# Optimization experiments

Measured on AMD Instinct MI355X. Metric: run time of the kernel, lower is better.

The kernel has to match this reference:

```python
import jax, jax.numpy as jnp
import numpy as np

NUM_USERS = 50000
NUM_ITEMS = 50000
N_NODES = NUM_USERS + NUM_ITEMS
EMBED_DIM = 64
NUM_LAYERS = 2
NUM_EDGES = 3200000


def setup_inputs() -> dict:
    key = jax.random.key(0)
    ks = jax.random.split(key, 8)
    edge_index = jax.random.randint(ks[0], (2, NUM_EDGES), 0, N_NODES, dtype=jnp.int32)
    edge_weight = jax.random.uniform(ks[1], (NUM_EDGES,), dtype=jnp.float32)
    scale = 1.0 / np.sqrt(EMBED_DIM)
    user_emb = jax.random.normal(ks[2], (NUM_USERS, EMBED_DIM), dtype=jnp.float32)
    item_emb = jax.random.normal(ks[3], (NUM_ITEMS, EMBED_DIM), dtype=jnp.float32)
    W1 = jax.random.normal(ks[4], (EMBED_DIM, EMBED_DIM), dtype=jnp.float32) * scale
    b1 = jnp.zeros((EMBED_DIM,), dtype=jnp.float32)
    W2 = jax.random.normal(ks[5], (EMBED_DIM, EMBED_DIM), dtype=jnp.float32) * scale
    b2 = jnp.zeros((EMBED_DIM,), dtype=jnp.float32)
    return {"edge_index": edge_index, "edge_weight": edge_weight,
            "user_emb": user_emb, "item_emb": item_emb,
            "W1": W1, "b1": b1, "W2": W2, "b2": b2}


def _gcn_layer(x, edge_index, edge_weight, W, b):
    # message: x_j * w_e ; aggregate: scatter-add to target nodes
    src, dst = edge_index[0], edge_index[1]
    msgs = x[src] * edge_weight[:, None]              # [E, D]
    agg = jax.ops.segment_sum(msgs, dst, num_segments=N_NODES)  # [N, D]
    updated = (agg + x) * 0.5                          # residual average
    return updated @ W.T + b                           # nn.Linear


def reference(edge_index, edge_weight, user_emb, item_emb, W1, b1, W2, b2):
    x = jnp.concatenate([user_emb, item_emb], axis=0)  # [N, D]
    x = _gcn_layer(x, edge_index, edge_weight, W1, b1)
    x = _gcn_layer(x, edge_index, edge_weight, W2, b2)
    return x
```

## Files before the change

kernel.cpp:

```cpp
#include <hip/hip_runtime.h>

#define N_NODES 100000
#define NUM_U 50000
#define D 64
#define NUM_E 3200000
#define NB 391
#define PBLK 256
#define CHUNK (NUM_E / PBLK)

__device__ __forceinline__ float bf2f(unsigned short u) {
  return __uint_as_float((unsigned)u << 16);
}
__device__ __forceinline__ unsigned short f2bf(float f) {
  unsigned u = __float_as_uint(f);
  u += 0x7FFF + ((u >> 16) & 1);
  return (unsigned short)(u >> 16);
}

__global__ __launch_bounds__(256) void micro_kernel(
    const float* __restrict__ W1, const float* __restrict__ W2,
    const float* __restrict__ b1, const float* __restrict__ b2,
    float* __restrict__ M, float* __restrict__ c, float* __restrict__ cc) {
  __shared__ float w1[64][65], w2[64][65];
  int t = (int)threadIdx.x;
  for (int i = t; i < 4096; i += 256) { w1[i >> 6][i & 63] = W1[i]; w2[i >> 6][i & 63] = W2[i]; }
  __syncthreads();
  for (int i = t; i < 4096; i += 256) {
    int k = i >> 6, j = i & 63;
    float s = 0.f;
#pragma unroll
    for (int tt = 0; tt < 64; ++tt) s = fmaf(w2[j][tt], w1[tt][k], s);
    M[i] = s;
  }
  if (t < 64) {
    float s = 0.f;
#pragma unroll
    for (int tt = 0; tt < 64; ++tt) s = fmaf(b1[tt], w2[t][tt], s);
    c[t] = s;
    cc[t] = 0.5f * s + b2[t];
  }
}

__global__ __launch_bounds__(256) void zmm_kernel(
    const float* __restrict__ xu, const float* __restrict__ xi,
    const float* __restrict__ M, unsigned short* __restrict__ z16) {
  __shared__ float Mt[64][65];
  __shared__ float U[64][65];
  int t = (int)threadIdx.x;
  for (int i = t; i < 4096; i += 256) Mt[i & 63][i >> 6] = M[i];
  int lane = t & 63, row = t >> 6;
  int n0 = (int)blockIdx.x * 64;
#pragma unroll
  for (int i = 0; i < 16; ++i) {
    int nl = row + 4 * i, n = n0 + nl;
    if (n < N_NODES) {
      const float* xr = (n < NUM_U) ? (xu + (size_t)n * D) : (xi + (size_t)(n - NUM_U) * D);
      U[nl][lane] = xr[lane];
    }
  }
  __syncthreads();
#pragma unroll
  for (int i = 0; i < 16; ++i) {
    int nl = row + 4 * i, n = n0 + nl;
    if (n >= N_NODES) continue;
    float s = 0.f;
#pragma unroll
    for (int k = 0; k < 64; ++k) s = fmaf(U[nl][k], Mt[lane][k], s);
    z16[(size_t)n * D + lane] = f2bf(s);
  }
}

__global__ __launch_bounds__(256) void p1_hist(const int4* __restrict__ dst4,
                                               int* __restrict__ gcnt,
                                               int* __restrict__ tot) {
  __shared__ int h[NB];
  int t = (int)threadIdx.x, blk = (int)blockIdx.x;
  for (int i = t; i < NB; i += 256) h[i] = 0;
  __syncthreads();
  int base4 = blk * (CHUNK / 4);
  for (int i = t; i < CHUNK / 4; i += 256) {
    int4 d = dst4[base4 + i];
    atomicAdd(&h[d.x >> 8], 1); atomicAdd(&h[d.y >> 8], 1);
    atomicAdd(&h[d.z >> 8], 1); atomicAdd(&h[d.w >> 8], 1);
  }
  __syncthreads();
  for (int i = t; i < NB; i += 256) {
    gcnt[i * PBLK + blk] = h[i];
    atomicAdd(&tot[i], h[i]);
  }
}

__global__ __launch_bounds__(512) void p2_scan(const int* __restrict__ tot,
                                               int* __restrict__ bbase,
                                               int* __restrict__ rowptr) {
  __shared__ int ps[512];
  int t = (int)threadIdx.x;
  int v = (t < NB) ? tot[t] : 0;
  ps[t] = v;
  __syncthreads();
  for (int off = 1; off < 512; off <<= 1) {
    int a = (t >= off) ? ps[t - off] : 0;
    __syncthreads();
    ps[t] += a;
    __syncthreads();
  }
  if (t < NB) bbase[t] = ps[t] - v;
  if (t == 0) { bbase[NB] = NUM_E; rowptr[N_NODES] = NUM_E; }
}

__global__ __launch_bounds__(256) void p2_off(const int* __restrict__ gcnt,
                                              const int* __restrict__ bbase,
                                              int* __restrict__ off) {
  __shared__ int ps[256];
  int t = (int)threadIdx.x, b = (int)blockIdx.x;
  int v = gcnt[b * PBLK + t];
  ps[t] = v;
  __syncthreads();
  for (int o = 1; o < 256; o <<= 1) {
    int a = (t >= o) ? ps[t - o] : 0;
    __syncthreads();
    ps[t] += a;
    __syncthreads();
  }
  off[b * PBLK + t] = bbase[b] + ps[t] - v;
}

__global__ __launch_bounds__(256) void p3_part(const int4* __restrict__ src4,
                                               const int4* __restrict__ dst4,
                                               const float4* __restrict__ w4,
                                               const int* __restrict__ off,
                                               int2* __restrict__ staging) {
  __shared__ int cur[NB];
  int t = (int)threadIdx.x, blk = (int)blockIdx.x;
  for (int i = t; i < NB; i += 256) cur[i] = off[i * PBLK + blk];
  __syncthreads();
  int base4 = blk * (CHUNK / 4);
  for (int i = t; i < CHUNK / 4; i += 256) {
    int4 s = src4[base4 + i];
    int4 d = dst4[base4 + i];
    float4 w = w4[base4 + i];
    int p;
    p = atomicAdd(&cur[d.x >> 8], 1);
    staging[p] = make_int2(s.x | ((d.x & 255) << 17), __float_as_int(w.x));
    p = atomicAdd(&cur[d.y >> 8], 1);
    staging[p] = make_int2(s.y | ((d.y & 255) << 17), __float_as_int(w.y));
    p = atomicAdd(&cur[d.z >> 8], 1);
    staging[p] = make_int2(s.z | ((d.z & 255) << 17), __float_as_int(w.z));
    p = atomicAdd(&cur[d.w >> 8], 1);
    staging[p] = make_int2(s.w | ((d.w & 255) << 17), __float_as_int(w.w));
  }
}

__global__ __launch_bounds__(256) void csr_finalize(
    const int* __restrict__ bbase, const int2* __restrict__ staging,
    int2* __restrict__ meta, int* __restrict__ rowptr) {
  __shared__ int hist[256];
  __shared__ int ps[256];
  __shared__ int cur[256];
  int t = (int)threadIdx.x, b = (int)blockIdx.x;
  int bs = bbase[b], be = bbase[b + 1];
  hist[t] = 0;
  __syncthreads();
  for (int i = bs + t; i < be; i += 256) atomicAdd(&hist[staging[i].x >> 17], 1);
  __syncthreads();
  int v = hist[t];
  ps[t] = v;
  __syncthreads();
  for (int o = 1; o < 256; o <<= 1) {
    int a = (t >= o) ? ps[t - o] : 0;
    __syncthreads();
    ps[t] += a;
    __syncthreads();
  }
  int base = bs + ps[t] - v;
  cur[t] = base;
  int n = b * 256 + t;
  if (n < N_NODES) rowptr[n] = base;
  __syncthreads();
  for (int i = bs + t; i < be; i += 256) {
    int2 m = staging[i];
    int dl = m.x >> 17;
    int p = atomicAdd(&cur[dl], 1);
    meta[p] = make_int2(m.x & 0x1FFFF, m.y);
  }
}

template <bool FINAL>
__global__ __launch_bounds__(256) void gather_kernel(
    const int* __restrict__ rowptr, const int2* __restrict__ meta,
    const unsigned short* __restrict__ gsrc, const unsigned short* __restrict__ z16,
    const float* __restrict__ c, const float* __restrict__ cc,
    float* __restrict__ outf, unsigned short* __restrict__ out16) {
  int t = (int)threadIdx.x, lane = t & 63;
  int wid = (int)((blockIdx.x * blockDim.x + t) >> 6);
  int nw = (int)((gridDim.x * blockDim.x) >> 6);
  float cl = FINAL ? c[lane] : 0.f;
  float ccl = FINAL ? cc[lane] : 0.f;

  for (int n = wid; n < N_NODES; n += nw) {
    int lo = __builtin_amdgcn_readfirstlane(rowptr[n]);
    int hi = __builtin_amdgcn_readfirstlane(rowptr[n + 1]);
    float acc0 = 0.f, acc1 = 0.f, wsum = 0.f;
    int j = lo;
    for (; j + 8 <= hi; j += 8) {
      int2 m0 = meta[j + 0], m1 = meta[j + 1], m2 = meta[j + 2], m3 = meta[j + 3];
      int2 m4 = meta[j + 4], m5 = meta[j + 5], m6 = meta[j + 6], m7 = meta[j + 7];
      float v0 = bf2f(gsrc[((size_t)m0.x << 6) + lane]);
      float v1 = bf2f(gsrc[((size_t)m1.x << 6) + lane]);
      float v2 = bf2f(gsrc[((size_t)m2.x << 6) + lane]);
      float v3 = bf2f(gsrc[((size_t)m3.x << 6) + lane]);
      float v4 = bf2f(gsrc[((size_t)m4.x << 6) + lane]);
      float v5 = bf2f(gsrc[((size_t)m5.x << 6) + lane]);
      float v6 = bf2f(gsrc[((size_t)m6.x << 6) + lane]);
      float v7 = bf2f(gsrc[((size_t)m7.x << 6) + lane]);
      acc0 = fmaf(v0, __int_as_float(m0.y), acc0);
      acc1 = fmaf(v1, __int_as_float(m1.y), acc1);
      acc0 = fmaf(v2, __int_as_float(m2.y), acc0);
      acc1 = fmaf(v3, __int_as_float(m3.y), acc1);
      acc0 = fmaf(v4, __int_as_float(m4.y), acc0);
      acc1 = fmaf(v5, __int_as_float(m5.y), acc1);
      acc0 = fmaf(v6, __int_as_float(m6.y), acc0);
      acc1 = fmaf(v7, __int_as_float(m7.y), acc1);
      if (FINAL) {
        float wa = (__int_as_float(m0.y) + __int_as_float(m1.y)) +
                   (__int_as_float(m2.y) + __int_as_float(m3.y));
        float wb = (__int_as_float(m4.y) + __int_as_float(m5.y)) +
                   (__int_as_float(m6.y) + __int_as_float(m7.y));
        wsum += wa + wb;
      }
    }
    for (; j < hi; ++j) {
      int2 m = meta[j];
      acc0 = fmaf(bf2f(gsrc[((size_t)m.x << 6) + lane]), __int_as_float(m.y), acc0);
      if (FINAL) wsum += __int_as_float(m.y);
    }
    float acc = acc0 + acc1;
    size_t o = ((size_t)n << 6) + lane;
    if (FINAL) {
      float t1n = bf2f(gsrc[o]);
      float zn = bf2f(z16[o]);
      outf[o] = 0.25f * acc + 0.5f * t1n + 0.25f * zn + 0.5f * wsum * cl + ccl;
    } else {
      out16[o] = f2bf(acc);
    }
  }
}

extern "C" void kernel_launch(void* const* d_in, const int* in_sizes, int n_in,
                              void* d_out, int out_size, void* d_ws, size_t ws_size,
                              hipStream_t stream) {
  const int* edge_index = (const int*)d_in[0];
  const int* src = edge_index;
  const int* dst = edge_index + NUM_E;
  const float* w = (const float*)d_in[1];
  const float* user_emb = (const float*)d_in[2];
  const float* item_emb = (const float*)d_in[3];
  const float* W1 = (const float*)d_in[4];
  const float* b1 = (const float*)d_in[5];
  const float* W2 = (const float*)d_in[6];
  const float* b2 = (const float*)d_in[7];
  float* out = (float*)d_out;

  unsigned short* z16 = (unsigned short*)d_ws;
  int2* staging = (int2*)(z16 + (size_t)N_NODES * D);
  unsigned short* t1_16 = (unsigned short*)staging;
  int2* meta = staging + NUM_E;
  int* rowptr = (int*)(meta + NUM_E);
  int* gcnt = rowptr + 100352;
  int* off = gcnt + NB * PBLK;
  int* tot = off + NB * PBLK;
  int* bbase = tot + 392;
  float* Mbuf = (float*)(bbase + 392);
  float* cbuf = Mbuf + 4096;
  float* ccbuf = cbuf + 64;

  hipMemsetAsync(tot, 0, NB * sizeof(int), stream);

  micro_kernel<<<1, 256, 0, stream>>>(W1, W2, b1, b2, Mbuf, cbuf, ccbuf);
  zmm_kernel<<<(N_NODES + 63) / 64, 256, 0, stream>>>(user_emb, item_emb, Mbuf, z16);

  p1_hist<<<PBLK, 256, 0, stream>>>((const int4*)dst, gcnt, tot);
  p2_scan<<<1, 512, 0, stream>>>(tot, bbase, rowptr);
  p2_off<<<NB, 256, 0, stream>>>(gcnt, bbase, off);
  p3_part<<<PBLK, 256, 0, stream>>>((const int4*)src, (const int4*)dst,
                                    (const float4*)w, off, staging);
  csr_finalize<<<NB, 256, 0, stream>>>(bbase, staging, meta, rowptr);

  gather_kernel<false><<<2048, 256, 0, stream>>>(rowptr, meta, z16, z16, cbuf,
                                                 ccbuf, nullptr, t1_16);
  gather_kernel<true><<<2048, 256, 0, stream>>>(rowptr, meta, t1_16, z16, cbuf,
                                                ccbuf, out, nullptr);
}
```

Measured before the change: 415.0 us.

## Stage partition and CSR scatter through LDS, drop per-block offset scan

The partition kernel now builds a local histogram and scan per block, sorts its chunk into shared memory, reserves global bucket ranges through atomic cursors, and writes contiguous runs to staging. This replaces the separate per-block count matrix and its offset-scan kernel. csr_finalize also sorts each bucket in LDS when it fits, then writes meta coalesced. The gather loop is unrolled to 16 loads in flight. The change removes scattered global writes and one kernel launch, at the cost of heavy LDS use per block (lower occupancy) and nondeterministic edge order within buckets.

```diff
diff --git a/kernel.cpp b/kernel.cpp
--- a/kernel.cpp
+++ b/kernel.cpp
@@ -5,8 +5,10 @@
 #define D 64
 #define NUM_E 3200000
 #define NB 391
-#define PBLK 256
+#define PBLK 500
 #define CHUNK (NUM_E / PBLK)
+#define CHUNK4 (CHUNK / 4)
+#define FCAP 8928
 
 __device__ __forceinline__ float bf2f(unsigned short u) {
   return __uint_as_float((unsigned)u << 16);
@@ -71,94 +73,108 @@
 }
 
 __global__ __launch_bounds__(256) void p1_hist(const int4* __restrict__ dst4,
-                                               int* __restrict__ gcnt,
                                                int* __restrict__ tot) {
   __shared__ int h[NB];
   int t = (int)threadIdx.x, blk = (int)blockIdx.x;
   for (int i = t; i < NB; i += 256) h[i] = 0;
   __syncthreads();
-  int base4 = blk * (CHUNK / 4);
-  for (int i = t; i < CHUNK / 4; i += 256) {
+  int base4 = blk * CHUNK4;
+  for (int i = t; i < CHUNK4; i += 256) {
     int4 d = dst4[base4 + i];
     atomicAdd(&h[d.x >> 8], 1); atomicAdd(&h[d.y >> 8], 1);
     atomicAdd(&h[d.z >> 8], 1); atomicAdd(&h[d.w >> 8], 1);
   }
   __syncthreads();
-  for (int i = t; i < NB; i += 256) {
-    gcnt[i * PBLK + blk] = h[i];
-    atomicAdd(&tot[i], h[i]);
-  }
+  for (int i = t; i < NB; i += 256)
+    if (h[i]) atomicAdd(&tot[i], h[i]);
 }
 
 __global__ __launch_bounds__(512) void p2_scan(const int* __restrict__ tot,
                                                int* __restrict__ bbase,
+                                               int* __restrict__ gcursor,
                                                int* __restrict__ rowptr) {
   __shared__ int ps[512];
   int t = (int)threadIdx.x;
   int v = (t < NB) ? tot[t] : 0;
   ps[t] = v;
   __syncthreads();
-  for (int off = 1; off < 512; off <<= 1) {
-    int a = (t >= off) ? ps[t - off] : 0;
+  for (int o = 1; o < 512; o <<= 1) {
+    int a = (t >= o) ? ps[t - o] : 0;
     __syncthreads();
     ps[t] += a;
     __syncthreads();
   }
-  if (t < NB) bbase[t] = ps[t] - v;
+  if (t < NB) { int e = ps[t] - v; bbase[t] = e; gcursor[t] = e; }
   if (t == 0) { bbase[NB] = NUM_E; rowptr[N_NODES] = NUM_E; }
 }
 
-__global__ __launch_bounds__(256) void p2_off(const int* __restrict__ gcnt,
-                                              const int* __restrict__ bbase,
-                                              int* __restrict__ off) {
-  __shared__ int ps[256];
-  int t = (int)threadIdx.x, b = (int)blockIdx.x;
-  int v = gcnt[b * PBLK + t];
-  ps[t] = v;
-  __syncthreads();
-  for (int o = 1; o < 256; o <<= 1) {
-    int a = (t >= o) ? ps[t - o] : 0;
-    __syncthreads();
-    ps[t] += a;
-    __syncthreads();
-  }
-  off[b * PBLK + t] = bbase[b] + ps[t] - v;
-}
-
-__global__ __launch_bounds__(256) void p3_part(const int4* __restrict__ src4,
+__global__ __launch_bounds__(512) void p3_part(const int4* __restrict__ src4,
                                                const int4* __restrict__ dst4,
                                                const float4* __restrict__ w4,
-                                               const int* __restrict__ off,
+                                               int* __restrict__ gcursor,
                                                int2* __restrict__ staging) {
-  __shared__ int cur[NB];
+  __shared__ int2 ent[CHUNK];
+  __shared__ int h[NB];
+  __shared__ int lst[NB + 1];
+  __shared__ int og[NB];
+  __shared__ int ps[512];
   int t = (int)threadIdx.x, blk = (int)blockIdx.x;
-  for (int i = t; i < NB; i += 256) cur[i] = off[i * PBLK + blk];
-  __syncthreads();
-  int base4 = blk * (CHUNK / 4);
-  for (int i = t; i < CHUNK / 4; i += 256) {
+  for (int i = t; i < NB; i += 512) h[i] = 0;
+  __syncthreads();
+  int base4 = blk * CHUNK4;
+  for (int i = t; i < CHUNK4; i += 512) {
+    int4 d = dst4[base4 + i];
+    atomicAdd(&h[d.x >> 8], 1); atomicAdd(&h[d.y >> 8], 1);
+    atomicAdd(&h[d.z >> 8], 1); atomicAdd(&h[d.w >> 8], 1);
+  }
+  __syncthreads();
+  int v = (t < NB) ? h[t] : 0;
+  ps[t] = v;
+  __syncthreads();
+  for (int o = 1; o < 512; o <<= 1) {
+    int a = (t >= o) ? ps[t - o] : 0;
+    __syncthreads();
+    ps[t] += a;
+    __syncthreads();
+  }
+  if (t < NB) {
+    lst[t] = ps[t] - v;
+    og[t] = v ? atomicAdd(&gcursor[t], v) : 0;
+  }
+  if (t == 0) lst[NB] = CHUNK;
+  __syncthreads();
+  if (t < NB) h[t] = lst[t];
+  __syncthreads();
+  for (int i = t; i < CHUNK4; i += 512) {
     int4 s = src4[base4 + i];
     int4 d = dst4[base4 + i];
     float4 w = w4[base4 + i];
     int p;
-    p = atomicAdd(&cur[d.x >> 8], 1);
-    staging[p] = make_int2(s.x | ((d.x & 255) << 17), __float_as_int(w.x));
-    p = atomicAdd(&cur[d.y >> 8], 1);
-    staging[p] = make_int2(s.y | ((d.y & 255) << 17), __float_as_int(w.y));
-    p = atomicAdd(&cur[d.z >> 8], 1);
-    staging[p] = make_int2(s.z | ((d.z & 255) << 17), __float_as_int(w.z));
-    p = atomicAdd(&cur[d.w >> 8], 1);
-    staging[p] = make_int2(s.w | ((d.w & 255) << 17), __float_as_int(w.w));
+    p = atomicAdd(&h[d.x >> 8], 1);
+    ent[p] = make_int2(s.x | ((d.x & 255) << 17), __float_as_int(w.x));
+    p = atomicAdd(&h[d.y >> 8], 1);
+    ent[p] = make_int2(s.y | ((d.y & 255) << 17), __float_as_int(w.y));
+    p = atomicAdd(&h[d.z >> 8], 1);
+    ent[p] = make_int2(s.z | ((d.z & 255) << 17), __float_as_int(w.z));
+    p = atomicAdd(&h[d.w >> 8], 1);
+    ent[p] = make_int2(s.w | ((d.w & 255) << 17), __float_as_int(w.w));
+  }
+  __syncthreads();
+  for (int i = t; i < CHUNK; i += 512) {
+    int lo = 0, hi = NB;
+    while (hi - lo > 1) { int mid = (lo + hi) >> 1; if (lst[mid] <= i) lo = mid; else hi = mid; }
+    staging[og[lo] + (i - lst[lo])] = ent[i];
   }
 }
 
 __global__ __launch_bounds__(256) void csr_finalize(
     const int* __restrict__ bbase, const int2* __restrict__ staging,
     int2* __restrict__ meta, int* __restrict__ rowptr) {
-  __shared__ int hist[256];
-  __shared__ int ps[256];
-  __shared__ int cur[256];
+  __shared__ int2 ent[FCAP];
+  __shared__ int hist[256], ps[256], cur[256];
   int t = (int)threadIdx.x, b = (int)blockIdx.x;
   int bs = bbase[b], be = bbase[b + 1];
+  int cnt = be - bs;
   hist[t] = 0;
   __syncthreads();
   for (int i = bs + t; i < be; i += 256) atomicAdd(&hist[staging[i].x >> 17], 1);
@@ -172,16 +188,27 @@
     ps[t] += a;
     __syncthreads();
   }
-  int base = bs + ps[t] - v;
-  cur[t] = base;
+  int lexcl = ps[t] - v;
   int n = b * 256 + t;
-  if (n < N_NODES) rowptr[n] = base;
-  __syncthreads();
-  for (int i = bs + t; i < be; i += 256) {
-    int2 m = staging[i];
-    int dl = m.x >> 17;
-    int p = atomicAdd(&cur[dl], 1);
-    meta[p] = make_int2(m.x & 0x1FFFF, m.y);
+  if (n < N_NODES) rowptr[n] = bs + lexcl;
+  if (cnt <= FCAP) {
+    cur[t] = lexcl;
+    __syncthreads();
+    for (int i = bs + t; i < be; i += 256) {
+      int2 m = staging[i];
+      int p = atomicAdd(&cur[m.x >> 17], 1);
+      ent[p] = make_int2(m.x & 0x1FFFF, m.y);
+    }
+    __syncthreads();
+    for (int i = t; i < cnt; i += 256) meta[bs + i] = ent[i];
+  } else {
+    cur[t] = bs + lexcl;
+    __syncthreads();
+    for (int i = bs + t; i < be; i += 256) {
+      int2 m = staging[i];
+      int p = atomicAdd(&cur[m.x >> 17], 1);
+      meta[p] = make_int2(m.x & 0x1FFFF, m.y);
+    }
   }
 }
 
@@ -202,32 +229,41 @@
     int hi = __builtin_amdgcn_readfirstlane(rowptr[n + 1]);
     float acc0 = 0.f, acc1 = 0.f, wsum = 0.f;
     int j = lo;
-    for (; j + 8 <= hi; j += 8) {
+    for (; j + 16 <= hi; j += 16) {
+      int2 mm[16];
+      float vv[16];
+#pragma unroll
+      for (int q = 0; q < 16; ++q) mm[q] = meta[j + q];
+#pragma unroll
+      for (int q = 0; q < 16; ++q) vv[q] = bf2f(gsrc[((size_t)mm[q].x << 6) + lane]);
+#pragma unroll
+      for (int q = 0; q < 16; ++q) {
+        if (q & 1) acc1 = fmaf(vv[q], __int_as_float(mm[q].y), acc1);
+        else       acc0 = fmaf(vv[q], __int_as_float(mm[q].y), acc0);
+      }
+      if (FINAL) {
+        float s0 = 0.f, s1 = 0.f;
+#pragma unroll
+        for (int q = 0; q < 16; q += 2) {
+          s0 += __int_as_float(mm[q].y);
+          s1 += __int_as_float(mm[q + 1].y);
+        }
+        wsum += s0 + s1;
+      }
+    }
+    for (; j + 4 <= hi; j += 4) {
       int2 m0 = meta[j + 0], m1 = meta[j + 1], m2 = meta[j + 2], m3 = meta[j + 3];
-      int2 m4 = meta[j + 4], m5 = meta[j + 5], m6 = meta[j + 6], m7 = meta[j + 7];
       float v0 = bf2f(gsrc[((size_t)m0.x << 6) + lane]);
       float v1 = bf2f(gsrc[((size_t)m1.x << 6) + lane]);
       float v2 = bf2f(gsrc[((size_t)m2.x << 6) + lane]);
       float v3 = bf2f(gsrc[((size_t)m3.x << 6) + lane]);
-      float v4 = bf2f(gsrc[((size_t)m4.x << 6) + lane]);
-      float v5 = bf2f(gsrc[((size_t)m5.x << 6) + lane]);
-      float v6 = bf2f(gsrc[((size_t)m6.x << 6) + lane]);
-      float v7 = bf2f(gsrc[((size_t)m7.x << 6) + lane]);
       acc0 = fmaf(v0, __int_as_float(m0.y), acc0);
       acc1 = fmaf(v1, __int_as_float(m1.y), acc1);
       acc0 = fmaf(v2, __int_as_float(m2.y), acc0);
       acc1 = fmaf(v3, __int_as_float(m3.y), acc1);
-      acc0 = fmaf(v4, __int_as_float(m4.y), acc0);
-      acc1 = fmaf(v5, __int_as_float(m5.y), acc1);
-      acc0 = fmaf(v6, __int_as_float(m6.y), acc0);
-      acc1 = fmaf(v7, __int_as_float(m7.y), acc1);
-      if (FINAL) {
-        float wa = (__int_as_float(m0.y) + __int_as_float(m1.y)) +
-                   (__int_as_float(m2.y) + __int_as_float(m3.y));
-        float wb = (__int_as_float(m4.y) + __int_as_float(m5.y)) +
-                   (__int_as_float(m6.y) + __int_as_float(m7.y));
-        wsum += wa + wb;
-      }
+      if (FINAL)
+        wsum += (__int_as_float(m0.y) + __int_as_float(m1.y)) +
+                (__int_as_float(m2.y) + __int_as_float(m3.y));
     }
     for (; j < hi; ++j) {
       int2 m = meta[j];
@@ -266,11 +302,10 @@
   unsigned short* t1_16 = (unsigned short*)staging;
   int2* meta = staging + NUM_E;
   int* rowptr = (int*)(meta + NUM_E);
-  int* gcnt = rowptr + 100352;
-  int* off = gcnt + NB * PBLK;
-  int* tot = off + NB * PBLK;
+  int* tot = rowptr + 100352;
   int* bbase = tot + 392;
-  float* Mbuf = (float*)(bbase + 392);
+  int* gcursor = bbase + 392;
+  float* Mbuf = (float*)(gcursor + 392);
   float* cbuf = Mbuf + 4096;
   float* ccbuf = cbuf + 64;
 
@@ -279,11 +314,10 @@
   micro_kernel<<<1, 256, 0, stream>>>(W1, W2, b1, b2, Mbuf, cbuf, ccbuf);
   zmm_kernel<<<(N_NODES + 63) / 64, 256, 0, stream>>>(user_emb, item_emb, Mbuf, z16);
 
-  p1_hist<<<PBLK, 256, 0, stream>>>((const int4*)dst, gcnt, tot);
-  p2_scan<<<1, 512, 0, stream>>>(tot, bbase, rowptr);
-  p2_off<<<NB, 256, 0, stream>>>(gcnt, bbase, off);
-  p3_part<<<PBLK, 256, 0, stream>>>((const int4*)src, (const int4*)dst,
-                                    (const float4*)w, off, staging);
+  p1_hist<<<PBLK, 256, 0, stream>>>((const int4*)dst, tot);
+  p2_scan<<<1, 512, 0, stream>>>(tot, bbase, gcursor, rowptr);
+  p3_part<<<PBLK, 512, 0, stream>>>((const int4*)src, (const int4*)dst,
+                                    (const float4*)w, gcursor, staging);
   csr_finalize<<<NB, 256, 0, stream>>>(bbase, staging, meta, rowptr);
 
   gather_kernel<false><<<2048, 256, 0, stream>>>(rowptr, meta, z16, z16, cbuf,
```

New measurement: 413.7 us. No clear change (-0.3%).
